# Kernel tuning notes

Hardware: AMD Instinct MI355X
Metric: run time of the kernel (lower is better)

Reference implementation:

```python
import jax, jax.numpy as jnp
import numpy as np
from jax import lax

DILATIONS = [1, 2, 4, 8, 16, 32, 64, 128, 256, 512]
KERNEL = 3
CH = 64
B, T = 8, 16384
L = len(DILATIONS)


def setup_inputs() -> dict:
    key = jax.random.key(0)
    ks = jax.random.split(key, 5)
    x = jax.random.normal(ks[0], (B, CH, T), dtype=jnp.float32)
    # gated conv: out_channels = 2*CH (tanh half | sigmoid half)
    weights_conv = jax.random.normal(ks[1], (L, 2 * CH, CH, KERNEL), dtype=jnp.float32) * 0.1
    biases_conv = jax.random.normal(ks[2], (L, 2 * CH), dtype=jnp.float32) * 0.1
    weights_out = jax.random.normal(ks[3], (L, CH, CH), dtype=jnp.float32) * 0.1
    biases_out = jax.random.normal(ks[4], (L, CH), dtype=jnp.float32) * 0.1
    return {
        "x": x,
        "weights_conv": weights_conv,
        "biases_conv": biases_conv,
        "weights_out": weights_out,
        "biases_out": biases_out,
    }


def _stack_forward(x, weights_conv, biases_conv, weights_out, biases_out):
    skips = []
    for i, d in enumerate(DILATIONS):
        h = x  # residual branch
        pad = (KERNEL - 1) * d  # causal left padding
        y = lax.conv_general_dilated(
            x, weights_conv[i],
            window_strides=(1,), padding=[(pad, 0)], rhs_dilation=(d,),
            dimension_numbers=("NCH", "OIH", "NCH"),
        ) + biases_conv[i][None, :, None]
        yt, ys = jnp.split(y, 2, axis=1)          # gated activation
        a = jnp.tanh(yt) * jax.nn.sigmoid(ys)      # (B, CH, T)
        skips.append(a)                            # skip = activation output
        if i < L - 1:  # last layer has use_output_transform=False
            out = jnp.einsum("oc,bct->bot", weights_out[i], a) + biases_out[i][None, :, None]
        else:
            out = a
        x = out + h  # residual add
    # pack (output, skips[0..L-1]) into one array of shape (L+1, B, CH, T)
    return jnp.concatenate([x[None], jnp.stack(skips, axis=0)], axis=0)


def reference(x, weights_conv, biases_conv, weights_out, biases_out):
    return _stack_forward(x, weights_conv, biases_conv, weights_out, biases_out)
```

## Files before the change

kernel.cpp:

```cpp
#include <hip/hip_runtime.h>
#include <hip/hip_bf16.h>


#define CH 64
#define TLEN 16384
#define NB 8
#define BN 128
#define NLAYER 10

typedef __attribute__((ext_vector_type(4))) float f32x4;
typedef __attribute__((ext_vector_type(8))) short s16x8;
typedef __attribute__((ext_vector_type(4))) unsigned short u16x4;

__device__ __forceinline__ unsigned short f2bf(float f) {
    union { float f; unsigned u; } v; v.f = f;
    unsigned r = v.u + 0x7fffu + ((v.u >> 16) & 1u);
    return (unsigned short)(r >> 16);
}
__device__ __forceinline__ float bf2f(unsigned short u) {
    union { unsigned u; float f; } v; v.u = ((unsigned)u) << 16;
    return v.f;
}
__device__ __forceinline__ void gload_lds16(const void* g, void* l) {
    __builtin_amdgcn_global_load_lds(
        (const __attribute__((address_space(1))) unsigned int*)g,
        (__attribute__((address_space(3))) unsigned int*)l, 16, 0, 0);
}

#define NCONV (NLAYER * 4 * 2 * 6 * 64 * 8)
#define NOUT  (NLAYER * 4 * 2 * 64 * 8)

__global__ void pack_weights(const float* __restrict__ wconv,
                             const float* __restrict__ wout,
                             unsigned short* __restrict__ wcpk,
                             unsigned short* __restrict__ wopk)
{
    int idx = blockIdx.x * 256 + threadIdx.x;
    if (idx < NCONV) {
        int j = idx & 7, t = idx >> 3;
        int lane = t & 63; t >>= 6;
        int ks = t % 6;   t /= 6;
        int m  = t & 1;   t >>= 1;
        int wv = t & 3;   int l = t >> 2;
        int o  = (m * 4 + wv) * 16 + (lane & 15);
        int ck = ks * 32 + (lane >> 4) * 8 + j;
        int kk = ck >> 6, c = ck & 63;
        wcpk[idx] = f2bf(wconv[(((size_t)l * 128 + o) * CH + c) * 3 + (2 - kk)]);
    } else if (idx < NCONV + NOUT) {
        int id = idx - NCONV;
        int j = id & 7, t = id >> 3;
        int lane = t & 63; t >>= 6;
        int ks = t & 1;    t >>= 1;
        int wv = t & 3;    int l = t >> 2;
        int o  = wv * 16 + (lane & 15);
        int c  = ks * 32 + (lane >> 4) * 8 + j;
        wopk[id] = f2bf(wout[((size_t)l * CH + o) * CH + c]);
    }
}

template<int I0, bool SRC_F32>
__global__ __launch_bounds__(256, 4)
void wavenet_pair(const void* __restrict__ xin_,
                  unsigned short* __restrict__ xoutp,
                  float* __restrict__ out,
                  const unsigned short* __restrict__ wcpk,
                  const unsigned short* __restrict__ wopk,
                  const float* __restrict__ bconv,
                  const float* __restrict__ bout)
{
    constexpr int d   = 1 << I0;
    constexpr int D   = 2 * d;
    constexpr int TD  = 2 * D;
    constexpr int W1T = (128 + TD + 15) / 16;
    constexpr int W1  = W1T * 16;
    constexpr int WIN = W1 + 2 * d;

    __shared__ __align__(16) unsigned short xs[WIN * 64];
    __shared__ __align__(16) unsigned short ci[W1 * 64];
    __shared__ __align__(16) unsigned short as2[64 * 64];

    const int tid  = threadIdx.x;
    const int lane = tid & 63;
    const int wv   = tid >> 6;
    const int hrow = lane & 15;
    const int kgrp = lane >> 4;
    const int b  = blockIdx.y;
    const int t0 = blockIdx.x * BN;
    const size_t xbase  = (size_t)b * CH * TLEN;
    const size_t planeF = (size_t)NB * CH * TLEN;
    const int o0 = wv * 16 + kgrp * 4;
    const int lo = t0 - 6 * d;

    if (SRC_F32) {
        const float* x = (const float*)xin_;
        #pragma unroll
        for (int c8 = 0; c8 < 8; ++c8) {
            for (int p = tid; p < WIN; p += 256) {
                const int tt = lo + p;
                s16x8 pk = {0, 0, 0, 0, 0, 0, 0, 0};
                if (tt >= 0 && tt < TLEN) {
                    const float* pp = x + xbase + (size_t)(c8 * 8) * TLEN + tt;
                    #pragma unroll
                    for (int j = 0; j < 8; ++j) pk[j] = (short)f2bf(pp[(size_t)j * TLEN]);
                }
                *reinterpret_cast<s16x8*>(&xs[(size_t)(c8 * WIN + p) * 8]) = pk;
            }
        }
    } else {
        const unsigned short* xb = (const unsigned short*)xin_ + xbase;
        constexpr int cnt = (WIN + 63) / 64;
        if (lo >= 0 && lo + WIN <= TLEN) {
            for (int task = wv; task < 8 * cnt; task += 4) {
                const int c8 = task / cnt, n0 = (task % cnt) * 64;
                const int rem = WIN - n0;
                const unsigned short* sp = xb + (size_t)(lo + n0 + lane) * CH + c8 * 8;
                unsigned short* dp = &xs[(size_t)(c8 * WIN + n0) * 8];
                if (rem >= 64) gload_lds16(sp, dp);
                else if (lane < rem) gload_lds16(sp, dp);
            }
        } else {
            for (int task = wv; task < 8 * cnt; task += 4) {
                const int c8 = task / cnt, n0 = (task % cnt) * 64;
                const int p = n0 + lane;
                if (p < WIN) {
                    const int tt = lo + p;
                    s16x8 pk = {0, 0, 0, 0, 0, 0, 0, 0};
                    if (tt >= 0 && tt < TLEN)
                        pk = *reinterpret_cast<const s16x8*>(xb + (size_t)tt * CH + c8 * 8);
                    *reinterpret_cast<s16x8*>(&xs[(size_t)(c8 * WIN + p) * 8]) = pk;
                }
            }
        }
    }

    s16x8 w0[6], w1[6], wa2[2];
    float bt[4], bs[4], bo[4];
    auto loadw = [&](int L) {
        const unsigned short* bw = wcpk + ((size_t)(L * 4 + wv) * 768 + lane) * 8;
        #pragma unroll
        for (int ks = 0; ks < 6; ++ks) {
            w0[ks] = *reinterpret_cast<const s16x8*>(bw + (size_t)ks * 512);
            w1[ks] = *reinterpret_cast<const s16x8*>(bw + (size_t)(6 + ks) * 512);
        }
        const unsigned short* b2 = wopk + ((size_t)(L * 4 + wv) * 128 + lane) * 8;
        wa2[0] = *reinterpret_cast<const s16x8*>(b2);
        wa2[1] = *reinterpret_cast<const s16x8*>(b2 + 512);
        const float* Bc = bconv + (size_t)L * 128;
        const float* Bo = bout + (size_t)L * CH;
        #pragma unroll
        for (int r = 0; r < 4; ++r) {
            bt[r] = Bc[o0 + r];
            bs[r] = Bc[64 + o0 + r];
            bo[r] = Bo[o0 + r];
        }
    };

    loadw(I0);
    __syncthreads();

    float* skipA = out + (size_t)(1 + I0) * planeF + xbase;
    #pragma unroll 1
    for (int c0 = 0; c0 < W1T; c0 += 3) {
        f32x4 aT[3], aS[3];
        #pragma unroll
        for (int i3 = 0; i3 < 3; ++i3) {
            aT[i3] = (f32x4){0.f, 0.f, 0.f, 0.f};
            aS[i3] = (f32x4){0.f, 0.f, 0.f, 0.f};
        }
        #pragma unroll
        for (int i3 = 0; i3 < 3; ++i3) {
            const int q = (c0 + i3) * 16 + hrow;
            #pragma unroll
            for (int ks = 0; ks < 6; ++ks) {
                const int kb = ks * 4 + kgrp;
                const int kk = kb >> 3, c8i = kb & 7;
                const s16x8 bf = *reinterpret_cast<const s16x8*>(
                    &xs[(size_t)(c8i * WIN + q + (2 - kk) * d) * 8]);
                aT[i3] = __builtin_amdgcn_mfma_f32_16x16x32_bf16(w0[ks], bf, aT[i3], 0, 0, 0);
                aS[i3] = __builtin_amdgcn_mfma_f32_16x16x32_bf16(w1[ks], bf, aS[i3], 0, 0, 0);
            }
        }
        #pragma unroll
        for (int i3 = 0; i3 < 3; ++i3) {
            const int q = (c0 + i3) * 16 + hrow;
            #pragma unroll
            for (int r = 0; r < 4; ++r) {
                const float yt = aT[i3][r] + bt[r];
                const float ys = aS[i3][r] + bs[r];
                const float th = 2.f * __builtin_amdgcn_rcpf(1.f + __expf(-2.f * yt)) - 1.f;
                const float sg = __builtin_amdgcn_rcpf(1.f + __expf(-ys));
                const float av = th * sg;
                const int c = o0 + r;
                if (q >= TD && q < TD + 128)
                    __builtin_nontemporal_store(av, &skipA[(size_t)c * TLEN + t0 + q - TD]);
                ci[(size_t)((c >> 3) * W1 + q) * 8 + (c & 7)] = f2bf(av);
            }
        }
        __syncthreads();
        u16x4 stash[3];
        #pragma unroll
        for (int i3 = 0; i3 < 3; ++i3) {
            const int q = (c0 + i3) * 16 + hrow;
            f32x4 acc = (f32x4){0.f, 0.f, 0.f, 0.f};
            #pragma unroll
            for (int ks2 = 0; ks2 < 2; ++ks2) {
                const s16x8 bf = *reinterpret_cast<const s16x8*>(
                    &ci[(size_t)((ks2 * 4 + kgrp) * W1 + q) * 8]);
                acc = __builtin_amdgcn_mfma_f32_16x16x32_bf16(wa2[ks2], bf, acc, 0, 0, 0);
            }
            const u16x4 rv = *reinterpret_cast<const u16x4*>(
                &xs[(size_t)((o0 >> 3) * WIN + q + 2 * d) * 8 + (o0 & 7)]);
            u16x4 ov;
            #pragma unroll
            for (int r = 0; r < 4; ++r)
                ov[r] = (t0 + q >= TD) ? f2bf(acc[r] + bo[r] + bf2f(rv[r]))
                                       : (unsigned short)0;
            stash[i3] = ov;
        }
        __syncthreads();
        #pragma unroll
        for (int i3 = 0; i3 < 3; ++i3) {
            const int q = (c0 + i3) * 16 + hrow;
            *reinterpret_cast<u16x4*>(&ci[(size_t)((o0 >> 3) * W1 + q) * 8 + (o0 & 7)]) = stash[i3];
        }
    }
    __syncthreads();

    loadw(I0 + 1);
    float* skipB = out + (size_t)(2 + I0) * planeF + xbase;
    unsigned short* xo = xoutp + xbase;

    #pragma unroll 1
    for (int hf = 0; hf < 2; ++hf) {
        f32x4 aT[4], aS[4];
        #pragma unroll
        for (int i4 = 0; i4 < 4; ++i4) {
            aT[i4] = (f32x4){0.f, 0.f, 0.f, 0.f};
            aS[i4] = (f32x4){0.f, 0.f, 0.f, 0.f};
        }
        #pragma unroll
        for (int i4 = 0; i4 < 4; ++i4) {
            const int n = (hf * 4 + i4) * 16 + hrow;
            #pragma unroll
            for (int ks = 0; ks < 6; ++ks) {
                const int kb = ks * 4 + kgrp;
                const int kk = kb >> 3, c8i = kb & 7;
                const s16x8 bf = *reinterpret_cast<const s16x8*>(
                    &ci[(size_t)(c8i * W1 + n + (2 - kk) * D) * 8]);
                aT[i4] = __builtin_amdgcn_mfma_f32_16x16x32_bf16(w0[ks], bf, aT[i4], 0, 0, 0);
                aS[i4] = __builtin_amdgcn_mfma_f32_16x16x32_bf16(w1[ks], bf, aS[i4], 0, 0, 0);
            }
        }
        #pragma unroll
        for (int i4 = 0; i4 < 4; ++i4) {
            const int n = (hf * 4 + i4) * 16 + hrow;
            #pragma unroll
            for (int r = 0; r < 4; ++r) {
                const float yt = aT[i4][r] + bt[r];
                const float ys = aS[i4][r] + bs[r];
                const float th = 2.f * __builtin_amdgcn_rcpf(1.f + __expf(-2.f * yt)) - 1.f;
                const float sg = __builtin_amdgcn_rcpf(1.f + __expf(-ys));
                const float av = th * sg;
                const int c = o0 + r;
                __builtin_nontemporal_store(av, &skipB[(size_t)c * TLEN + t0 + n]);
                as2[(size_t)((c >> 3) * 64 + (n - hf * 64)) * 8 + (c & 7)] = f2bf(av);
            }
        }
        __syncthreads();
        #pragma unroll
        for (int i4 = 0; i4 < 4; ++i4) {
            const int n = (hf * 4 + i4) * 16 + hrow;
            const int nl = n - hf * 64;
            f32x4 acc = (f32x4){0.f, 0.f, 0.f, 0.f};
            #pragma unroll
            for (int ks2 = 0; ks2 < 2; ++ks2) {
                const s16x8 bf = *reinterpret_cast<const s16x8*>(
                    &as2[(size_t)((ks2 * 4 + kgrp) * 64 + nl) * 8]);
                acc = __builtin_amdgcn_mfma_f32_16x16x32_bf16(wa2[ks2], bf, acc, 0, 0, 0);
            }
            const u16x4 rv = *reinterpret_cast<const u16x4*>(
                &ci[(size_t)((o0 >> 3) * W1 + n + TD) * 8 + (o0 & 7)]);
            u16x4 ov;
            #pragma unroll
            for (int r = 0; r < 4; ++r) ov[r] = f2bf(acc[r] + bo[r] + bf2f(rv[r]));
            *reinterpret_cast<u16x4*>(&xo[(size_t)(t0 + n) * CH + o0]) = ov;
        }
        __syncthreads();
    }
}

template<int SM, bool LAST>
__global__ __launch_bounds__(256, 3)
void wavenet_layer(const void* __restrict__ xin_, void* __restrict__ xout_,
                   float* __restrict__ skip,
                   const unsigned short* __restrict__ wcpk,
                   const unsigned short* __restrict__ wopk,
                   const float* __restrict__ bconv, const float* __restrict__ bout,
                   int layer, int dil)
{
    extern __shared__ __align__(16) unsigned short xs[];
    unsigned short* as_ = xs;

    const int tid  = threadIdx.x;
    const int lane = tid & 63;
    const int wv   = tid >> 6;
    const int hrow = lane & 15;
    const int kgrp = lane >> 4;
    const int b  = blockIdx.y;
    const int t0 = blockIdx.x * BN;
    const int NW = BN + 2 * dil;
    const size_t xbase = (size_t)b * CH * TLEN;

    if (SM == 1) {
        const unsigned short* xin = (const unsigned short*)xin_;
        const int cnt_n = (NW + 63) >> 6;
        if (t0 >= 2 * dil) {
            for (int ch = wv; ch < 8 * cnt_n; ch += 4) {
                const int c8 = ch / cnt_n;
                const int n0 = (ch % cnt_n) * 64;
                const int rem = NW - n0;
                const unsigned short* src =
                    xin + xbase + (size_t)(t0 - 2 * dil + n0 + lane) * CH + c8 * 8;
                unsigned short* dst = &xs[(size_t)(c8 * NW + n0) * 8];
                if (rem >= 64) gload_lds16(src, dst);
                else if (lane < rem) gload_lds16(src, dst);
            }
        } else {
            for (int ch = wv; ch < 8 * cnt_n; ch += 4) {
                const int c8 = ch / cnt_n;
                const int n0 = (ch % cnt_n) * 64;
                if (n0 + lane < NW) {
                    const int tg = t0 - 2 * dil + n0 + lane;
                    s16x8 pk = {0, 0, 0, 0, 0, 0, 0, 0};
                    if (tg >= 0)
                        pk = *reinterpret_cast<const s16x8*>(xin + xbase + (size_t)tg * CH + c8 * 8);
                    *reinterpret_cast<s16x8*>(&xs[(size_t)(c8 * NW + n0 + lane) * 8]) = pk;
                }
            }
        }
    } else {
        const unsigned short* xin = (const unsigned short*)xin_;
        if (t0 >= 2 * dil) {
            for (int ch = wv; ch < 48; ch += 4) {
                const int kk = ch >> 4, c8 = (ch >> 1) & 7, n0 = (ch & 1) * 64;
                const unsigned short* src =
                    xin + xbase + (size_t)(t0 + n0 + lane - kk * dil) * CH + c8 * 8;
                unsigned short* dst = &xs[(size_t)((kk * 8 + c8) * BN + n0) * 8];
                gload_lds16(src, dst);
            }
        } else {
            for (int ch = wv; ch < 48; ch += 4) {
                const int kk = ch >> 4, c8 = (ch >> 1) & 7, n0 = (ch & 1) * 64;
                const int tg = t0 + n0 + lane - kk * dil;
                s16x8 pk = {0, 0, 0, 0, 0, 0, 0, 0};
                if (tg >= 0)
                    pk = *reinterpret_cast<const s16x8*>(xin + xbase + (size_t)tg * CH + c8 * 8);
                *reinterpret_cast<s16x8*>(&xs[(size_t)((kk * 8 + c8) * BN + n0 + lane) * 8]) = pk;
            }
        }
    }

    s16x8 w0[6], w1[6];
    {
        const unsigned short* basew = wcpk + ((size_t)(layer * 4 + wv) * 768 + lane) * 8;
        #pragma unroll
        for (int ks = 0; ks < 6; ++ks) {
            w0[ks] = *reinterpret_cast<const s16x8*>(basew + (size_t)ks * 512);
            w1[ks] = *reinterpret_cast<const s16x8*>(basew + (size_t)(6 + ks) * 512);
        }
    }
    const float* Bc = bconv + (size_t)layer * 128;
    float bt[4], bs[4];
    #pragma unroll
    for (int r = 0; r < 4; ++r) {
        bt[r] = Bc[wv * 16 + kgrp * 4 + r];
        bs[r] = Bc[64 + wv * 16 + kgrp * 4 + r];
    }

    __syncthreads();

    f32x4 accT[8], accS[8];
    #pragma unroll
    for (int nt = 0; nt < 8; ++nt) {
        accT[nt] = (f32x4){0.f, 0.f, 0.f, 0.f};
        accS[nt] = (f32x4){0.f, 0.f, 0.f, 0.f};
    }
    #pragma unroll
    for (int nt = 0; nt < 8; ++nt) {
        #pragma unroll
        for (int ks = 0; ks < 6; ++ks) {
            const int kb = ks * 4 + kgrp;
            const unsigned short* bp;
            if (SM == 2) {
                bp = &xs[(size_t)(kb * BN + nt * 16 + hrow) * 8];
            } else {
                const int kk = kb >> 3, c8i = kb & 7;
                bp = &xs[(size_t)(c8i * NW + nt * 16 + hrow + (2 - kk) * dil) * 8];
            }
            const s16x8 bf = *reinterpret_cast<const s16x8*>(bp);
            accT[nt] = __builtin_amdgcn_mfma_f32_16x16x32_bf16(w0[ks], bf, accT[nt], 0, 0, 0);
            accS[nt] = __builtin_amdgcn_mfma_f32_16x16x32_bf16(w1[ks], bf, accS[nt], 0, 0, 0);
        }
    }

    if (!LAST) __syncthreads();

    #pragma unroll
    for (int nt = 0; nt < 8; ++nt) {
        #pragma unroll
        for (int r = 0; r < 4; ++r) {
            const float yt = accT[nt][r] + bt[r];
            const float ys = accS[nt][r] + bs[r];
            const float th = 2.f * __builtin_amdgcn_rcpf(1.f + __expf(-2.f * yt)) - 1.f;
            const float sg = __builtin_amdgcn_rcpf(1.f + __expf(-ys));
            const float av = th * sg;
            const int c = wv * 16 + kgrp * 4 + r;
            const int n = nt * 16 + hrow;
            __builtin_nontemporal_store(av, &skip[xbase + (size_t)c * TLEN + t0 + n]);
            if (LAST) {
                const float res = bf2f(xs[(size_t)((c >> 3) * BN + n) * 8 + (c & 7)]);
                __builtin_nontemporal_store(av + res,
                    &((float*)xout_)[xbase + (size_t)c * TLEN + t0 + n]);
            } else {
                as_[(size_t)((c >> 3) * BN + n) * 8 + (c & 7)] = f2bf(av);
            }
        }
    }

    if (LAST) return;

    __syncthreads();

    s16x8 wa2[2];
    {
        const unsigned short* b2 = wopk + ((size_t)(layer * 4 + wv) * 128 + lane) * 8;
        wa2[0] = *reinterpret_cast<const s16x8*>(b2);
        wa2[1] = *reinterpret_cast<const s16x8*>(b2 + 512);
    }
    const float* Bo = bout + (size_t)layer * CH;
    float bo[4];
    #pragma unroll
    for (int r = 0; r < 4; ++r) bo[r] = Bo[wv * 16 + kgrp * 4 + r];

    const int o0 = wv * 16 + kgrp * 4;
    unsigned short* xout = (unsigned short*)xout_;

    #pragma unroll
    for (int nt = 0; nt < 8; ++nt) {
        f32x4 acc = (f32x4){0.f, 0.f, 0.f, 0.f};
        #pragma unroll
        for (int ks = 0; ks < 2; ++ks) {
            const s16x8 bf = *reinterpret_cast<const s16x8*>(
                &as_[(size_t)((ks * 4 + kgrp) * BN + nt * 16 + hrow) * 8]);
            acc = __builtin_amdgcn_mfma_f32_16x16x32_bf16(wa2[ks], bf, acc, 0, 0, 0);
        }
        const int n = nt * 16 + hrow;
        const u16x4 rv = *reinterpret_cast<const u16x4*>(
            (const unsigned short*)xin_ + xbase + (size_t)(t0 + n) * CH + o0);
        u16x4 ov;
        #pragma unroll
        for (int r = 0; r < 4; ++r) ov[r] = f2bf(acc[r] + bo[r] + bf2f(rv[r]));
        *reinterpret_cast<u16x4*>(&xout[xbase + (size_t)(t0 + n) * CH + o0]) = ov;
    }
}

extern "C" void kernel_launch(void* const* d_in, const int* in_sizes, int n_in,
                              void* d_out, int out_size, void* d_ws, size_t ws_size,
                              hipStream_t stream)
{
    const float* x  = (const float*)d_in[0];
    const float* wc = (const float*)d_in[1];
    const float* bc = (const float*)d_in[2];
    const float* wo = (const float*)d_in[3];
    const float* bo = (const float*)d_in[4];
    float* out = (float*)d_out;
    const size_t planeF = (size_t)NB * CH * TLEN;

    unsigned short* PA = (unsigned short*)d_ws;
    unsigned short* PB = PA + planeF;
    unsigned short* wcpk = PB + planeF;
    unsigned short* wopk = wcpk + NCONV;

    pack_weights<<<(NCONV + NOUT) / 256, 256, 0, stream>>>(wc, wo, wcpk, wopk);

    dim3 grid(TLEN / BN, NB), block(256);

    wavenet_pair<0, true ><<<grid, block, 0, stream>>>(x,  PA, out, wcpk, wopk, bc, bo);
    wavenet_pair<2, false><<<grid, block, 0, stream>>>(PA, PB, out, wcpk, wopk, bc, bo);
    wavenet_pair<4, false><<<grid, block, 0, stream>>>(PB, PA, out, wcpk, wopk, bc, bo);

    wavenet_layer<1, false><<<grid, block, (size_t)(BN + 128) * 128, stream>>>(
        PA, PB, out + 7 * planeF, wcpk, wopk, bc, bo, 6, 64);
    wavenet_layer<2, false><<<grid, block, 24 * BN * 8 * 2, stream>>>(
        PB, PA, out + 8 * planeF, wcpk, wopk, bc, bo, 7, 128);
    wavenet_layer<2, false><<<grid, block, 24 * BN * 8 * 2, stream>>>(
        PA, PB, out + 9 * planeF, wcpk, wopk, bc, bo, 8, 256);
    wavenet_layer<2, true><<<grid, block, 24 * BN * 8 * 2, stream>>>(
        PB, out, out + 10 * planeF, wcpk, wopk, bc, bo, 9, 512);
}
```

Before: 233.8 us.

## Process two time tiles per block with XCD swizzle and prefetched staging

```diff
diff --git a/kernel.cpp b/kernel.cpp
--- a/kernel.cpp
+++ b/kernel.cpp
@@ -25,6 +25,13 @@
     __builtin_amdgcn_global_load_lds(
         (const __attribute__((address_space(1))) unsigned int*)g,
         (__attribute__((address_space(3))) unsigned int*)l, 16, 0, 0);
+}
+__device__ __forceinline__ void swz2(int& pi, int& b) {
+    const int lin = blockIdx.y * 64 + blockIdx.x;
+    const int xcd = lin & 7;
+    const int idx = lin >> 3;
+    pi = xcd * 8 + (idx & 7);
+    b  = idx >> 3;
 }
 
 #define NCONV (NLAYER * 4 * 2 * 6 * 64 * 8)
@@ -84,54 +91,11 @@
     const int wv   = tid >> 6;
     const int hrow = lane & 15;
     const int kgrp = lane >> 4;
-    const int b  = blockIdx.y;
-    const int t0 = blockIdx.x * BN;
+    int pi, b;
+    swz2(pi, b);
     const size_t xbase  = (size_t)b * CH * TLEN;
     const size_t planeF = (size_t)NB * CH * TLEN;
     const int o0 = wv * 16 + kgrp * 4;
-    const int lo = t0 - 6 * d;
-
-    if (SRC_F32) {
-        const float* x = (const float*)xin_;
-        #pragma unroll
-        for (int c8 = 0; c8 < 8; ++c8) {
-            for (int p = tid; p < WIN; p += 256) {
-                const int tt = lo + p;
-                s16x8 pk = {0, 0, 0, 0, 0, 0, 0, 0};
-                if (tt >= 0 && tt < TLEN) {
-                    const float* pp = x + xbase + (size_t)(c8 * 8) * TLEN + tt;
-                    #pragma unroll
-                    for (int j = 0; j < 8; ++j) pk[j] = (short)f2bf(pp[(size_t)j * TLEN]);
-                }
-                *reinterpret_cast<s16x8*>(&xs[(size_t)(c8 * WIN + p) * 8]) = pk;
-            }
-        }
-    } else {
-        const unsigned short* xb = (const unsigned short*)xin_ + xbase;
-        constexpr int cnt = (WIN + 63) / 64;
-        if (lo >= 0 && lo + WIN <= TLEN) {
-            for (int task = wv; task < 8 * cnt; task += 4) {
-                const int c8 = task / cnt, n0 = (task % cnt) * 64;
-                const int rem = WIN - n0;
-                const unsigned short* sp = xb + (size_t)(lo + n0 + lane) * CH + c8 * 8;
-                unsigned short* dp = &xs[(size_t)(c8 * WIN + n0) * 8];
-                if (rem >= 64) gload_lds16(sp, dp);
-                else if (lane < rem) gload_lds16(sp, dp);
-            }
-        } else {
-            for (int task = wv; task < 8 * cnt; task += 4) {
-                const int c8 = task / cnt, n0 = (task % cnt) * 64;
-                const int p = n0 + lane;
-                if (p < WIN) {
-                    const int tt = lo + p;
-                    s16x8 pk = {0, 0, 0, 0, 0, 0, 0, 0};
-                    if (tt >= 0 && tt < TLEN)
-                        pk = *reinterpret_cast<const s16x8*>(xb + (size_t)tt * CH + c8 * 8);
-                    *reinterpret_cast<s16x8*>(&xs[(size_t)(c8 * WIN + p) * 8]) = pk;
-                }
-            }
-        }
-    }
 
     s16x8 w0[6], w1[6], wa2[2];
     float bt[4], bs[4], bo[4];
@@ -155,312 +119,354 @@
         }
     };
 
-    loadw(I0);
-    __syncthreads();
-
-    float* skipA = out + (size_t)(1 + I0) * planeF + xbase;
+    auto stage_window = [&](int lo) {
+        if (SRC_F32) {
+            const float* x = (const float*)xin_;
+            #pragma unroll
+            for (int c8 = 0; c8 < 8; ++c8) {
+                for (int q0 = tid; q0 < WIN; q0 += 256) {
+                    const int tt = lo + q0;
+                    s16x8 pk = {0, 0, 0, 0, 0, 0, 0, 0};
+                    if (tt >= 0 && tt < TLEN) {
+                        const float* pp = x + xbase + (size_t)(c8 * 8) * TLEN + tt;
+                        #pragma unroll
+                        for (int j = 0; j < 8; ++j) pk[j] = (short)f2bf(pp[(size_t)j * TLEN]);
+                    }
+                    *reinterpret_cast<s16x8*>(&xs[(size_t)(c8 * WIN + q0) * 8]) = pk;
+                }
+            }
+        } else {
+            const unsigned short* xb = (const unsigned short*)xin_ + xbase;
+            constexpr int cnt = (WIN + 63) / 64;
+            if (lo >= 0 && lo + WIN <= TLEN) {
+                for (int task = wv; task < 8 * cnt; task += 4) {
+                    const int c8 = task / cnt, n0 = (task % cnt) * 64;
+                    const int rem = WIN - n0;
+                    const unsigned short* sp = xb + (size_t)(lo + n0 + lane) * CH + c8 * 8;
+                    unsigned short* dp = &xs[(size_t)(c8 * WIN + n0) * 8];
+                    if (rem >= 64) gload_lds16(sp, dp);
+                    else if (lane < rem) gload_lds16(sp, dp);
+                }
+            } else {
+                for (int task = wv; task < 8 * cnt; task += 4) {
+                    const int c8 = task / cnt, n0 = (task % cnt) * 64;
+                    const int q0 = n0 + lane;
+                    if (q0 < WIN) {
+                        const int tt = lo + q0;
+                        s16x8 pk = {0, 0, 0, 0, 0, 0, 0, 0};
+                        if (tt >= 0 && tt < TLEN)
+                            pk = *reinterpret_cast<const s16x8*>(xb + (size_t)tt * CH + c8 * 8);
+                        *reinterpret_cast<s16x8*>(&xs[(size_t)(c8 * WIN + q0) * 8]) = pk;
+                    }
+                }
+            }
+        }
+    };
+
     #pragma unroll 1
-    for (int c0 = 0; c0 < W1T; c0 += 3) {
-        f32x4 aT[3], aS[3];
-        #pragma unroll
-        for (int i3 = 0; i3 < 3; ++i3) {
-            aT[i3] = (f32x4){0.f, 0.f, 0.f, 0.f};
-            aS[i3] = (f32x4){0.f, 0.f, 0.f, 0.f};
-        }
-        #pragma unroll
-        for (int i3 = 0; i3 < 3; ++i3) {
-            const int q = (c0 + i3) * 16 + hrow;
-            #pragma unroll
-            for (int ks = 0; ks < 6; ++ks) {
-                const int kb = ks * 4 + kgrp;
-                const int kk = kb >> 3, c8i = kb & 7;
-                const s16x8 bf = *reinterpret_cast<const s16x8*>(
-                    &xs[(size_t)(c8i * WIN + q + (2 - kk) * d) * 8]);
-                aT[i3] = __builtin_amdgcn_mfma_f32_16x16x32_bf16(w0[ks], bf, aT[i3], 0, 0, 0);
-                aS[i3] = __builtin_amdgcn_mfma_f32_16x16x32_bf16(w1[ks], bf, aS[i3], 0, 0, 0);
-            }
-        }
-        #pragma unroll
-        for (int i3 = 0; i3 < 3; ++i3) {
-            const int q = (c0 + i3) * 16 + hrow;
-            #pragma unroll
-            for (int r = 0; r < 4; ++r) {
-                const float yt = aT[i3][r] + bt[r];
-                const float ys = aS[i3][r] + bs[r];
-                const float th = 2.f * __builtin_amdgcn_rcpf(1.f + __expf(-2.f * yt)) - 1.f;
-                const float sg = __builtin_amdgcn_rcpf(1.f + __expf(-ys));
-                const float av = th * sg;
-                const int c = o0 + r;
-                if (q >= TD && q < TD + 128)
-                    __builtin_nontemporal_store(av, &skipA[(size_t)c * TLEN + t0 + q - TD]);
-                ci[(size_t)((c >> 3) * W1 + q) * 8 + (c & 7)] = f2bf(av);
+    for (int sub = 0; sub < 2; ++sub) {
+        const int t0 = (2 * pi + sub) * BN;
+        const int lo = t0 - 6 * d;
+        if (sub == 0) stage_window(lo);
+        loadw(I0);
+        if (sub == 0) __syncthreads();
+
+        float* skipA = out + (size_t)(1 + I0) * planeF + xbase;
+        #pragma unroll 1
+        for (int c0 = 0; c0 < W1T; c0 += 3) {
+            f32x4 aT[3], aS[3];
+            #pragma unroll
+            for (int i3 = 0; i3 < 3; ++i3) {
+                aT[i3] = (f32x4){0.f, 0.f, 0.f, 0.f};
+                aS[i3] = (f32x4){0.f, 0.f, 0.f, 0.f};
+            }
+            #pragma unroll
+            for (int i3 = 0; i3 < 3; ++i3) {
+                const int q = (c0 + i3) * 16 + hrow;
+                #pragma unroll
+                for (int ks = 0; ks < 6; ++ks) {
+                    const int kb = ks * 4 + kgrp;
+                    const int kk = kb >> 3, c8i = kb & 7;
+                    const s16x8 bf = *reinterpret_cast<const s16x8*>(
+                        &xs[(size_t)(c8i * WIN + q + (2 - kk) * d) * 8]);
+                    aT[i3] = __builtin_amdgcn_mfma_f32_16x16x32_bf16(w0[ks], bf, aT[i3], 0, 0, 0);
+                    aS[i3] = __builtin_amdgcn_mfma_f32_16x16x32_bf16(w1[ks], bf, aS[i3], 0, 0, 0);
+                }
+            }
+            #pragma unroll
+            for (int i3 = 0; i3 < 3; ++i3) {
+                const int q = (c0 + i3) * 16 + hrow;
+                #pragma unroll
+                for (int r = 0; r < 4; ++r) {
+                    const float yt = aT[i3][r] + bt[r];
+                    const float ys = aS[i3][r] + bs[r];
+                    const float th = 2.f * __builtin_amdgcn_rcpf(1.f + __expf(-2.f * yt)) - 1.f;
+                    const float sg = __builtin_amdgcn_rcpf(1.f + __expf(-ys));
+                    const float av = th * sg;
+                    const int c = o0 + r;
+                    if (q >= TD && q < TD + 128)
+                        __builtin_nontemporal_store(av, &skipA[(size_t)c * TLEN + t0 + q - TD]);
+                    ci[(size_t)((c >> 3) * W1 + q) * 8 + (c & 7)] = f2bf(av);
+                }
+            }
+            __syncthreads();
+            u16x4 stash[3];
+            #pragma unroll
+            for (int i3 = 0; i3 < 3; ++i3) {
+                const int q = (c0 + i3) * 16 + hrow;
+                f32x4 acc = (f32x4){0.f, 0.f, 0.f, 0.f};
+                #pragma unroll
+                for (int ks2 = 0; ks2 < 2; ++ks2) {
+                    const s16x8 bf = *reinterpret_cast<const s16x8*>(
+                        &ci[(size_t)((ks2 * 4 + kgrp) * W1 + q) * 8]);
+                    acc = __builtin_amdgcn_mfma_f32_16x16x32_bf16(wa2[ks2], bf, acc, 0, 0, 0);
+                }
+                const u16x4 rv = *reinterpret_cast<const u16x4*>(
+                    &xs[(size_t)((o0 >> 3) * WIN + q + 2 * d) * 8 + (o0 & 7)]);
+                u16x4 ov;
+                #pragma unroll
+                for (int r = 0; r < 4; ++r)
+                    ov[r] = (t0 + q >= TD) ? f2bf(acc[r] + bo[r] + bf2f(rv[r]))
+                                           : (unsigned short)0;
+                stash[i3] = ov;
+            }
+            __syncthreads();
+            #pragma unroll
+            for (int i3 = 0; i3 < 3; ++i3) {
+                const int q = (c0 + i3) * 16 + hrow;
+                *reinterpret_cast<u16x4*>(&ci[(size_t)((o0 >> 3) * W1 + q) * 8 + (o0 & 7)]) = stash[i3];
             }
         }
         __syncthreads();
-        u16x4 stash[3];
-        #pragma unroll
-        for (int i3 = 0; i3 < 3; ++i3) {
-            const int q = (c0 + i3) * 16 + hrow;
-            f32x4 acc = (f32x4){0.f, 0.f, 0.f, 0.f};
-            #pragma unroll
-            for (int ks2 = 0; ks2 < 2; ++ks2) {
-                const s16x8 bf = *reinterpret_cast<const s16x8*>(
-                    &ci[(size_t)((ks2 * 4 + kgrp) * W1 + q) * 8]);
-                acc = __builtin_amdgcn_mfma_f32_16x16x32_bf16(wa2[ks2], bf, acc, 0, 0, 0);
-            }
-            const u16x4 rv = *reinterpret_cast<const u16x4*>(
-                &xs[(size_t)((o0 >> 3) * WIN + q + 2 * d) * 8 + (o0 & 7)]);
-            u16x4 ov;
-            #pragma unroll
-            for (int r = 0; r < 4; ++r)
-                ov[r] = (t0 + q >= TD) ? f2bf(acc[r] + bo[r] + bf2f(rv[r]))
-                                       : (unsigned short)0;
-            stash[i3] = ov;
-        }
-        __syncthreads();
-        #pragma unroll
-        for (int i3 = 0; i3 < 3; ++i3) {
-            const int q = (c0 + i3) * 16 + hrow;
-            *reinterpret_cast<u16x4*>(&ci[(size_t)((o0 >> 3) * W1 + q) * 8 + (o0 & 7)]) = stash[i3];
+        if (sub == 0) stage_window(lo + BN);
+
+        loadw(I0 + 1);
+        float* skipB = out + (size_t)(2 + I0) * planeF + xbase;
+        unsigned short* xo = xoutp + xbase;
+
+        #pragma unroll 1
+        for (int hf = 0; hf < 2; ++hf) {
+            f32x4 aT[4], aS[4];
+            #pragma unroll
+            for (int i4 = 0; i4 < 4; ++i4) {
+                aT[i4] = (f32x4){0.f, 0.f, 0.f, 0.f};
+                aS[i4] = (f32x4){0.f, 0.f, 0.f, 0.f};
+            }
+            #pragma unroll
+            for (int i4 = 0; i4 < 4; ++i4) {
+                const int n = (hf * 4 + i4) * 16 + hrow;
+                #pragma unroll
+                for (int ks = 0; ks < 6; ++ks) {
+                    const int kb = ks * 4 + kgrp;
+                    const int kk = kb >> 3, c8i = kb & 7;
+                    const s16x8 bf = *reinterpret_cast<const s16x8*>(
+                        &ci[(size_t)(c8i * W1 + n + (2 - kk) * D) * 8]);
+                    aT[i4] = __builtin_amdgcn_mfma_f32_16x16x32_bf16(w0[ks], bf, aT[i4], 0, 0, 0);
+                    aS[i4] = __builtin_amdgcn_mfma_f32_16x16x32_bf16(w1[ks], bf, aS[i4], 0, 0, 0);
+                }
+            }
+            #pragma unroll
+            for (int i4 = 0; i4 < 4; ++i4) {
+                const int n = (hf * 4 + i4) * 16 + hrow;
+                #pragma unroll
+                for (int r = 0; r < 4; ++r) {
+                    const float yt = aT[i4][r] + bt[r];
+                    const float ys = aS[i4][r] + bs[r];
+                    const float th = 2.f * __builtin_amdgcn_rcpf(1.f + __expf(-2.f * yt)) - 1.f;
+                    const float sg = __builtin_amdgcn_rcpf(1.f + __expf(-ys));
+                    const float av = th * sg;
+                    const int c = o0 + r;
+                    __builtin_nontemporal_store(av, &skipB[(size_t)c * TLEN + t0 + n]);
+                    as2[(size_t)((c >> 3) * 64 + (n - hf * 64)) * 8 + (c & 7)] = f2bf(av);
+                }
+            }
+            __syncthreads();
+            #pragma unroll
+            for (int i4 = 0; i4 < 4; ++i4) {
+                const int n = (hf * 4 + i4) * 16 + hrow;
+                const int nl = n - hf * 64;
+                f32x4 acc = (f32x4){0.f, 0.f, 0.f, 0.f};
+                #pragma unroll
+                for (int ks2 = 0; ks2 < 2; ++ks2) {
+                    const s16x8 bf = *reinterpret_cast<const s16x8*>(
+                        &as2[(size_t)((ks2 * 4 + kgrp) * 64 + nl) * 8]);
+                    acc = __builtin_amdgcn_mfma_f32_16x16x32_bf16(wa2[ks2], bf, acc, 0, 0, 0);
+                }
+                const u16x4 rv = *reinterpret_cast<const u16x4*>(
+                    &ci[(size_t)((o0 >> 3) * W1 + n + TD) * 8 + (o0 & 7)]);
+                u16x4 ov;
+                #pragma unroll
+                for (int r = 0; r < 4; ++r) ov[r] = f2bf(acc[r] + bo[r] + bf2f(rv[r]));
+                *reinterpret_cast<u16x4*>(&xo[(size_t)(t0 + n) * CH + o0]) = ov;
+            }
+            __syncthreads();
         }
     }
-    __syncthreads();
-
-    loadw(I0 + 1);
-    float* skipB = out + (size_t)(2 + I0) * planeF + xbase;
-    unsigned short* xo = xoutp + xbase;
-
-    #pragma unroll 1
-    for (int hf = 0; hf < 2; ++hf) {
-        f32x4 aT[4], aS[4];
-        #pragma unroll
-        for (int i4 = 0; i4 < 4; ++i4) {
-            aT[i4] = (f32x4){0.f, 0.f, 0.f, 0.f};
-            aS[i4] = (f32x4){0.f, 0.f, 0.f, 0.f};
-        }
-        #pragma unroll
-        for (int i4 = 0; i4 < 4; ++i4) {
-            const int n = (hf * 4 + i4) * 16 + hrow;
-            #pragma unroll
-            for (int ks = 0; ks < 6; ++ks) {
-                const int kb = ks * 4 + kgrp;
-                const int kk = kb >> 3, c8i = kb & 7;
-                const s16x8 bf = *reinterpret_cast<const s16x8*>(
-                    &ci[(size_t)(c8i * W1 + n + (2 - kk) * D) * 8]);
-                aT[i4] = __builtin_amdgcn_mfma_f32_16x16x32_bf16(w0[ks], bf, aT[i4], 0, 0, 0);
-                aS[i4] = __builtin_amdgcn_mfma_f32_16x16x32_bf16(w1[ks], bf, aS[i4], 0, 0, 0);
-            }
-        }
-        #pragma unroll
-        for (int i4 = 0; i4 < 4; ++i4) {
-            const int n = (hf * 4 + i4) * 16 + hrow;
-            #pragma unroll
-            for (int r = 0; r < 4; ++r) {
-                const float yt = aT[i4][r] + bt[r];
-                const float ys = aS[i4][r] + bs[r];
-                const float th = 2.f * __builtin_amdgcn_rcpf(1.f + __expf(-2.f * yt)) - 1.f;
-                const float sg = __builtin_amdgcn_rcpf(1.f + __expf(-ys));
-                const float av = th * sg;
-                const int c = o0 + r;
-                __builtin_nontemporal_store(av, &skipB[(size_t)c * TLEN + t0 + n]);
-                as2[(size_t)((c >> 3) * 64 + (n - hf * 64)) * 8 + (c & 7)] = f2bf(av);
-            }
-        }
-        __syncthreads();
-        #pragma unroll
-        for (int i4 = 0; i4 < 4; ++i4) {
-            const int n = (hf * 4 + i4) * 16 + hrow;
-            const int nl = n - hf * 64;
-            f32x4 acc = (f32x4){0.f, 0.f, 0.f, 0.f};
-            #pragma unroll
-            for (int ks2 = 0; ks2 < 2; ++ks2) {
-                const s16x8 bf = *reinterpret_cast<const s16x8*>(
-                    &as2[(size_t)((ks2 * 4 + kgrp) * 64 + nl) * 8]);
-                acc = __builtin_amdgcn_mfma_f32_16x16x32_bf16(wa2[ks2], bf, acc, 0, 0, 0);
-            }
-            const u16x4 rv = *reinterpret_cast<const u16x4*>(
-                &ci[(size_t)((o0 >> 3) * W1 + n + TD) * 8 + (o0 & 7)]);
-            u16x4 ov;
-            #pragma unroll
-            for (int r = 0; r < 4; ++r) ov[r] = f2bf(acc[r] + bo[r] + bf2f(rv[r]));
-            *reinterpret_cast<u16x4*>(&xo[(size_t)(t0 + n) * CH + o0]) = ov;
-        }
-        __syncthreads();
-    }
 }
 
 template<int SM, bool LAST>
-__global__ __launch_bounds__(256, 3)
-void wavenet_layer(const void* __restrict__ xin_, void* __restrict__ xout_,
-                   float* __restrict__ skip,
-                   const unsigned short* __restrict__ wcpk,
-                   const unsigned short* __restrict__ wopk,
-                   const float* __restrict__ bconv, const float* __restrict__ bout,
-                   int layer, int dil)
+__global__ __launch_bounds__(256, (SM == 2 && !LAST) ? 2 : 3)
+void wavenet_tail(const unsigned short* __restrict__ xin, void* __restrict__ xout_,
+                  float* __restrict__ skip,
+                  const unsigned short* __restrict__ wcpk,
+                  const unsigned short* __restrict__ wopk,
+                  const float* __restrict__ bconv, const float* __restrict__ bout,
+                  int layer, int dil)
 {
-    extern __shared__ __align__(16) unsigned short xs[];
-    unsigned short* as_ = xs;
+    constexpr int XSN = (SM == 1) ? (8 * 256 * 8) : (24 * BN * 8);
+    __shared__ __align__(16) unsigned short xs[XSN];
+    __shared__ __align__(16) unsigned short as_[LAST ? 16 : (8 * BN * 8)];
 
     const int tid  = threadIdx.x;
     const int lane = tid & 63;
     const int wv   = tid >> 6;
     const int hrow = lane & 15;
     const int kgrp = lane >> 4;
-    const int b  = blockIdx.y;
-    const int t0 = blockIdx.x * BN;
-    const int NW = BN + 2 * dil;
+    int pi, b;
+    swz2(pi, b);
     const size_t xbase = (size_t)b * CH * TLEN;
-
-    if (SM == 1) {
-        const unsigned short* xin = (const unsigned short*)xin_;
-        const int cnt_n = (NW + 63) >> 6;
-        if (t0 >= 2 * dil) {
-            for (int ch = wv; ch < 8 * cnt_n; ch += 4) {
-                const int c8 = ch / cnt_n;
-                const int n0 = (ch % cnt_n) * 64;
-                const int rem = NW - n0;
-                const unsigned short* src =
-                    xin + xbase + (size_t)(t0 - 2 * dil + n0 + lane) * CH + c8 * 8;
-                unsigned short* dst = &xs[(size_t)(c8 * NW + n0) * 8];
-                if (rem >= 64) gload_lds16(src, dst);
-                else if (lane < rem) gload_lds16(src, dst);
-            }
-        } else {
-            for (int ch = wv; ch < 8 * cnt_n; ch += 4) {
-                const int c8 = ch / cnt_n;
-                const int n0 = (ch % cnt_n) * 64;
-                if (n0 + lane < NW) {
-                    const int tg = t0 - 2 * dil + n0 + lane;
-                    s16x8 pk = {0, 0, 0, 0, 0, 0, 0, 0};
-                    if (tg >= 0)
-                        pk = *reinterpret_cast<const s16x8*>(xin + xbase + (size_t)tg * CH + c8 * 8);
-                    *reinterpret_cast<s16x8*>(&xs[(size_t)(c8 * NW + n0 + lane) * 8]) = pk;
-                }
-            }
-        }
-    } else {
-        const unsigned short* xin = (const unsigned short*)xin_;
-        if (t0 >= 2 * dil) {
-            for (int ch = wv; ch < 48; ch += 4) {
-                const int kk = ch >> 4, c8 = (ch >> 1) & 7, n0 = (ch & 1) * 64;
-                const unsigned short* src =
-                    xin + xbase + (size_t)(t0 + n0 + lane - kk * dil) * CH + c8 * 8;
-                unsigned short* dst = &xs[(size_t)((kk * 8 + c8) * BN + n0) * 8];
-                gload_lds16(src, dst);
-            }
-        } else {
-            for (int ch = wv; ch < 48; ch += 4) {
-                const int kk = ch >> 4, c8 = (ch >> 1) & 7, n0 = (ch & 1) * 64;
-                const int tg = t0 + n0 + lane - kk * dil;
-                s16x8 pk = {0, 0, 0, 0, 0, 0, 0, 0};
-                if (tg >= 0)
-                    pk = *reinterpret_cast<const s16x8*>(xin + xbase + (size_t)tg * CH + c8 * 8);
-                *reinterpret_cast<s16x8*>(&xs[(size_t)((kk * 8 + c8) * BN + n0 + lane) * 8]) = pk;
-            }
-        }
-    }
-
-    s16x8 w0[6], w1[6];
+    const unsigned short* xb = xin + xbase;
+    const int o0 = wv * 16 + kgrp * 4;
+
+    s16x8 w0[6], w1[6], wa2[2];
     {
-        const unsigned short* basew = wcpk + ((size_t)(layer * 4 + wv) * 768 + lane) * 8;
+        const unsigned short* bw = wcpk + ((size_t)(layer * 4 + wv) * 768 + lane) * 8;
         #pragma unroll
         for (int ks = 0; ks < 6; ++ks) {
-            w0[ks] = *reinterpret_cast<const s16x8*>(basew + (size_t)ks * 512);
-            w1[ks] = *reinterpret_cast<const s16x8*>(basew + (size_t)(6 + ks) * 512);
-        }
-    }
-    const float* Bc = bconv + (size_t)layer * 128;
-    float bt[4], bs[4];
-    #pragma unroll
-    for (int r = 0; r < 4; ++r) {
-        bt[r] = Bc[wv * 16 + kgrp * 4 + r];
-        bs[r] = Bc[64 + wv * 16 + kgrp * 4 + r];
-    }
-
-    __syncthreads();
-
-    f32x4 accT[8], accS[8];
-    #pragma unroll
-    for (int nt = 0; nt < 8; ++nt) {
-        accT[nt] = (f32x4){0.f, 0.f, 0.f, 0.f};
-        accS[nt] = (f32x4){0.f, 0.f, 0.f, 0.f};
-    }
-    #pragma unroll
-    for (int nt = 0; nt < 8; ++nt) {
-        #pragma unroll
-        for (int ks = 0; ks < 6; ++ks) {
-            const int kb = ks * 4 + kgrp;
-            const unsigned short* bp;
-            if (SM == 2) {
-                bp = &xs[(size_t)(kb * BN + nt * 16 + hrow) * 8];
-            } else {
-                const int kk = kb >> 3, c8i = kb & 7;
-                bp = &xs[(size_t)(c8i * NW + nt * 16 + hrow + (2 - kk) * dil) * 8];
-            }
-            const s16x8 bf = *reinterpret_cast<const s16x8*>(bp);
-            accT[nt] = __builtin_amdgcn_mfma_f32_16x16x32_bf16(w0[ks], bf, accT[nt], 0, 0, 0);
-            accS[nt] = __builtin_amdgcn_mfma_f32_16x16x32_bf16(w1[ks], bf, accS[nt], 0, 0, 0);
-        }
-    }
-
-    if (!LAST) __syncthreads();
-
-    #pragma unroll
-    for (int nt = 0; nt < 8; ++nt) {
-        #pragma unroll
-        for (int r = 0; r < 4; ++r) {
-            const float yt = accT[nt][r] + bt[r];
-            const float ys = accS[nt][r] + bs[r];
-            const float th = 2.f * __builtin_amdgcn_rcpf(1.f + __expf(-2.f * yt)) - 1.f;
-            const float sg = __builtin_amdgcn_rcpf(1.f + __expf(-ys));
-            const float av = th * sg;
-            const int c = wv * 16 + kgrp * 4 + r;
-            const int n = nt * 16 + hrow;
-            __builtin_nontemporal_store(av, &skip[xbase + (size_t)c * TLEN + t0 + n]);
-            if (LAST) {
-                const float res = bf2f(xs[(size_t)((c >> 3) * BN + n) * 8 + (c & 7)]);
-                __builtin_nontemporal_store(av + res,
-                    &((float*)xout_)[xbase + (size_t)c * TLEN + t0 + n]);
-            } else {
-                as_[(size_t)((c >> 3) * BN + n) * 8 + (c & 7)] = f2bf(av);
-            }
-        }
-    }
-
-    if (LAST) return;
-
-    __syncthreads();
-
-    s16x8 wa2[2];
-    {
+            w0[ks] = *reinterpret_cast<const s16x8*>(bw + (size_t)ks * 512);
+            w1[ks] = *reinterpret_cast<const s16x8*>(bw + (size_t)(6 + ks) * 512);
+        }
         const unsigned short* b2 = wopk + ((size_t)(layer * 4 + wv) * 128 + lane) * 8;
         wa2[0] = *reinterpret_cast<const s16x8*>(b2);
         wa2[1] = *reinterpret_cast<const s16x8*>(b2 + 512);
     }
+    const float* Bc = bconv + (size_t)layer * 128;
     const float* Bo = bout + (size_t)layer * CH;
-    float bo[4];
+    float bt[4], bs[4], bo[4];
     #pragma unroll
-    for (int r = 0; r < 4; ++r) bo[r] = Bo[wv * 16 + kgrp * 4 + r];
-
-    const int o0 = wv * 16 + kgrp * 4;
-    unsigned short* xout = (unsigned short*)xout_;
-
-    #pragma unroll
-    for (int nt = 0; nt < 8; ++nt) {
-        f32x4 acc = (f32x4){0.f, 0.f, 0.f, 0.f};
+    for (int r = 0; r < 4; ++r) {
+        bt[r] = Bc[o0 + r];
+        bs[r] = Bc[64 + o0 + r];
+        bo[r] = Bo[o0 + r];
+    }
+
+    auto stage = [&](int t0) {
+        if (SM == 1) {
+            if (t0 >= 128) {
+                for (int task = wv; task < 32; task += 4) {
+                    const int c8 = task >> 2, n0 = (task & 3) * 64;
+                    gload_lds16(xb + (size_t)(t0 - 128 + n0 + lane) * CH + c8 * 8,
+                                &xs[(size_t)(c8 * 256 + n0) * 8]);
+                }
+            } else {
+                for (int task = wv; task < 32; task += 4) {
+                    const int c8 = task >> 2, n0 = (task & 3) * 64;
+                    const int tg = t0 - 128 + n0 + lane;
+                    s16x8 pk = {0, 0, 0, 0, 0, 0, 0, 0};
+                    if (tg >= 0)
+                        pk = *reinterpret_cast<const s16x8*>(xb + (size_t)tg * CH + c8 * 8);
+                    *reinterpret_cast<s16x8*>(&xs[(size_t)(c8 * 256 + n0 + lane) * 8]) = pk;
+                }
+            }
+        } else {
+            if (t0 >= 2 * dil) {
+                for (int ch = wv; ch < 48; ch += 4) {
+                    const int kk = ch >> 4, c8 = (ch >> 1) & 7, n0 = (ch & 1) * 64;
+                    gload_lds16(xb + (size_t)(t0 + n0 + lane - kk * dil) * CH + c8 * 8,
+                                &xs[(size_t)((kk * 8 + c8) * BN + n0) * 8]);
+                }
+            } else {
+                for (int ch = wv; ch < 48; ch += 4) {
+                    const int kk = ch >> 4, c8 = (ch >> 1) & 7, n0 = (ch & 1) * 64;
+                    const int tg = t0 + n0 + lane - kk * dil;
+                    s16x8 pk = {0, 0, 0, 0, 0, 0, 0, 0};
+                    if (tg >= 0)
+                        pk = *reinterpret_cast<const s16x8*>(xb + (size_t)tg * CH + c8 * 8);
+                    *reinterpret_cast<s16x8*>(&xs[(size_t)((kk * 8 + c8) * BN + n0 + lane) * 8]) = pk;
+                }
+            }
+        }
+    };
+
+    #pragma unroll 1
+    for (int sub = 0; sub < 2; ++sub) {
+        const int t0 = (2 * pi + sub) * BN;
+        if (sub == 0) { stage(t0); __syncthreads(); }
+
+        f32x4 accT[8], accS[8];
         #pragma unroll
-        for (int ks = 0; ks < 2; ++ks) {
-            const s16x8 bf = *reinterpret_cast<const s16x8*>(
-                &as_[(size_t)((ks * 4 + kgrp) * BN + nt * 16 + hrow) * 8]);
-            acc = __builtin_amdgcn_mfma_f32_16x16x32_bf16(wa2[ks], bf, acc, 0, 0, 0);
-        }
-        const int n = nt * 16 + hrow;
-        const u16x4 rv = *reinterpret_cast<const u16x4*>(
-            (const unsigned short*)xin_ + xbase + (size_t)(t0 + n) * CH + o0);
-        u16x4 ov;
+        for (int nt = 0; nt < 8; ++nt) {
+            accT[nt] = (f32x4){0.f, 0.f, 0.f, 0.f};
+            accS[nt] = (f32x4){0.f, 0.f, 0.f, 0.f};
+        }
         #pragma unroll
-        for (int r = 0; r < 4; ++r) ov[r] = f2bf(acc[r] + bo[r] + bf2f(rv[r]));
-        *reinterpret_cast<u16x4*>(&xout[xbase + (size_t)(t0 + n) * CH + o0]) = ov;
+        for (int nt = 0; nt < 8; ++nt) {
+            #pragma unroll
+            for (int ks = 0; ks < 6; ++ks) {
+                const int kb = ks * 4 + kgrp;
+                const unsigned short* bp;
+                if (SM == 2) {
+                    bp = &xs[(size_t)(kb * BN + nt * 16 + hrow) * 8];
+                } else {
+                    const int kk = kb >> 3, c8i = kb & 7;
+                    bp = &xs[(size_t)(c8i * 256 + nt * 16 + hrow + (2 - kk) * dil) * 8];
+                }
+                const s16x8 bf = *reinterpret_cast<const s16x8*>(bp);
+                accT[nt] = __builtin_amdgcn_mfma_f32_16x16x32_bf16(w0[ks], bf, accT[nt], 0, 0, 0);
+                accS[nt] = __builtin_amdgcn_mfma_f32_16x16x32_bf16(w1[ks], bf, accS[nt], 0, 0, 0);
+            }
+        }
+        u16x4 rvL[8];
+        if (LAST) {
+            #pragma unroll
+            for (int nt = 0; nt < 8; ++nt)
+                rvL[nt] = *reinterpret_cast<const u16x4*>(
+                    &xs[(size_t)((o0 >> 3) * BN + nt * 16 + hrow) * 8 + (o0 & 7)]);
+        }
+        __syncthreads();
+        if (sub == 0) stage(t0 + BN);
+
+        #pragma unroll
+        for (int nt = 0; nt < 8; ++nt) {
+            const int n = nt * 16 + hrow;
+            #pragma unroll
+            for (int r = 0; r < 4; ++r) {
+                const float yt = accT[nt][r] + bt[r];
+                const float ys = accS[nt][r] + bs[r];
+                const float th = 2.f * __builtin_amdgcn_rcpf(1.f + __expf(-2.f * yt)) - 1.f;
+                const float sg = __builtin_amdgcn_rcpf(1.f + __expf(-ys));
+                const float av = th * sg;
+                const int c = o0 + r;
+                __builtin_nontemporal_store(av, &skip[xbase + (size_t)c * TLEN + t0 + n]);
+                if (LAST) {
+                    __builtin_nontemporal_store(av + bf2f(rvL[nt][r]),
+                        &((float*)xout_)[xbase + (size_t)c * TLEN + t0 + n]);
+                } else {
+                    as_[(size_t)((c >> 3) * BN + n) * 8 + (c & 7)] = f2bf(av);
+                }
+            }
+        }
+        if (!LAST) {
+            __syncthreads();
+            unsigned short* xo = (unsigned short*)xout_ + xbase;
+            #pragma unroll
+            for (int nt = 0; nt < 8; ++nt) {
+                const int n = nt * 16 + hrow;
+                f32x4 acc = (f32x4){0.f, 0.f, 0.f, 0.f};
+                #pragma unroll
+                for (int ks = 0; ks < 2; ++ks) {
+                    const s16x8 bf = *reinterpret_cast<const s16x8*>(
+                        &as_[(size_t)((ks * 4 + kgrp) * BN + n) * 8]);
+                    acc = __builtin_amdgcn_mfma_f32_16x16x32_bf16(wa2[ks], bf, acc, 0, 0, 0);
+                }
+                const u16x4 rv = *reinterpret_cast<const u16x4*>(xb + (size_t)(t0 + n) * CH + o0);
+                u16x4 ov;
+                #pragma unroll
+                for (int r = 0; r < 4; ++r) ov[r] = f2bf(acc[r] + bo[r] + bf2f(rv[r]));
+                *reinterpret_cast<u16x4*>(&xo[(size_t)(t0 + n) * CH + o0]) = ov;
+            }
+        }
+        __syncthreads();
     }
 }
 
@@ -483,18 +489,18 @@
 
     pack_weights<<<(NCONV + NOUT) / 256, 256, 0, stream>>>(wc, wo, wcpk, wopk);
 
-    dim3 grid(TLEN / BN, NB), block(256);
-
-    wavenet_pair<0, true ><<<grid, block, 0, stream>>>(x,  PA, out, wcpk, wopk, bc, bo);
-    wavenet_pair<2, false><<<grid, block, 0, stream>>>(PA, PB, out, wcpk, wopk, bc, bo);
-    wavenet_pair<4, false><<<grid, block, 0, stream>>>(PB, PA, out, wcpk, wopk, bc, bo);
-
-    wavenet_layer<1, false><<<grid, block, (size_t)(BN + 128) * 128, stream>>>(
+    dim3 grid2(64, NB), block(256);
+
+    wavenet_pair<0, true ><<<grid2, block, 0, stream>>>(x,  PA, out, wcpk, wopk, bc, bo);
+    wavenet_pair<2, false><<<grid2, block, 0, stream>>>(PA, PB, out, wcpk, wopk, bc, bo);
+    wavenet_pair<4, false><<<grid2, block, 0, stream>>>(PB, PA, out, wcpk, wopk, bc, bo);
+
+    wavenet_tail<1, false><<<grid2, block, 0, stream>>>(
         PA, PB, out + 7 * planeF, wcpk, wopk, bc, bo, 6, 64);
-    wavenet_layer<2, false><<<grid, block, 24 * BN * 8 * 2, stream>>>(
+    wavenet_tail<2, false><<<grid2, block, 0, stream>>>(
         PB, PA, out + 8 * planeF, wcpk, wopk, bc, bo, 7, 128);
-    wavenet_layer<2, false><<<grid, block, 24 * BN * 8 * 2, stream>>>(
+    wavenet_tail<2, false><<<grid2, block, 0, stream>>>(
         PA, PB, out + 9 * planeF, wcpk, wopk, bc, bo, 8, 256);
-    wavenet_layer<2, true><<<grid, block, 24 * BN * 8 * 2, stream>>>(
+    wavenet_tail<2, true><<<grid2, block, 0, stream>>>(
         PB, out, out + 10 * planeF, wcpk, wopk, bc, bo, 9, 512);
 }
```

After: 278.8 us. 1.19x slower.
